# Kernel tuning notes

Measured on AMD Instinct MI355X. Metric: run time of the kernel, lower is better.

Reference implementation:

```python
import jax, jax.numpy as jnp
import numpy as np
from jax import lax

B, T, D, H = 4, 4096, 1024, 8
DK, DV = 1024, 2048          # expand_k=1.0, expand_v=2.0
RANK, MAXL, LOOPD = 16, 8, 128  # lora_rank, max_loops, dim*loop_dim_fraction
THRESH = 0.99
EPS = 1e-6
GK_SCALE = 16.0              # GLA forget-gate temperature


def setup_inputs() -> dict:
    key = jax.random.key(0)
    ks = jax.random.split(key, 16)
    r = lambda i, shape, s=0.02: jax.random.normal(ks[i], shape, jnp.float32) * s
    return {
        "h": jax.random.normal(ks[0], (B, T, D), jnp.float32),
        "e": jax.random.normal(ks[1], (B, T, D), jnp.float32),
        "norm_w": jnp.ones((D,), jnp.float32),
        "out_norm_w": jnp.ones((D,), jnp.float32),
        "Wq": r(2, (D, DK)), "Wk": r(3, (D, DK)), "Wv": r(4, (D, DV)),
        "Wgk": r(5, (D, DK)), "Wg": r(6, (D, DV)), "Wo": r(7, (DV, D)),
        "lora_A": r(8, (MAXL, D, RANK)), "lora_B": r(9, (MAXL, RANK, D)),
        "inj_A": 0.9 * jnp.eye(D, dtype=jnp.float32) + r(10, (D, D)),
        "inj_B": r(11, (D, D)),
        "act_w": r(12, (D,)),
        "act_b": jnp.full((), -2.0, jnp.float32),  # gradual halting
        "loop_table": r(13, (MAXL, LOOPD)),
        "n_loops": 4,
    }


def rmsnorm(x, w):
    return x * lax.rsqrt(jnp.mean(x * x, axis=-1, keepdims=True) + EPS) * w


def gla(x, Wq, Wk, Wv, Wgk, Wg, Wo, num_heads):
    """Gated Linear Attention: data-dependent forget gates, linear-time recurrent scan."""
    b, t, d = x.shape
    dk, dv = Wq.shape[1], Wv.shape[1]
    dkh, dvh = dk // num_heads, dv // num_heads
    q = (x @ Wq).reshape(b, t, num_heads, dkh) * (dkh ** -0.5)
    k = (x @ Wk).reshape(b, t, num_heads, dkh)
    v = (x @ Wv).reshape(b, t, num_heads, dvh)
    # forget gate alpha in (0,1): exp(logsigmoid(gk)/16)
    alpha = jnp.exp(jax.nn.log_sigmoid(x @ Wgk) / GK_SCALE).reshape(b, t, num_heads, dkh)

    def step(S, qkva):  # S: (b, H, dkh, dvh)
        qt, kt, vt, at = qkva
        S = at[..., None] * S + kt[..., None] * vt[..., None, :]
        ot = jnp.einsum('bhk,bhkv->bhv', qt, S)
        return S, ot

    S0 = jnp.zeros((b, num_heads, dkh, dvh), x.dtype)
    xs = (jnp.swapaxes(q, 0, 1), jnp.swapaxes(k, 0, 1),
          jnp.swapaxes(v, 0, 1), jnp.swapaxes(alpha, 0, 1))
    _, o = lax.scan(step, S0, xs)                  # o: (t, b, H, dvh)
    o = jnp.swapaxes(o, 0, 1).reshape(b, t, dv)
    o = o * jax.nn.silu(x @ Wg)                    # output gate
    return o @ Wo


def reference(h, e, norm_w, out_norm_w, Wq, Wk, Wv, Wgk, Wg, Wo,
              lora_A, lora_B, inj_A, inj_B, act_w, act_b, loop_table, n_loops):
    b, t_len, d = h.shape
    halted = jnp.zeros((b, t_len), bool)
    cum = jnp.zeros((b, t_len), h.dtype)
    h_out = jnp.zeros_like(h)
    loopd = loop_table.shape[1]
    for t in range(n_loops):  # small fixed depth loop (structurally distinct LoRA/embed per t)
        # loop index embedding on first loopd channels
        h = h.at[..., :loopd].add(loop_table[t])
        h_norm = rmsnorm(h + e, norm_w)
        g = gla(h_norm, Wq, Wk, Wv, Wgk, Wg, Wo, H)   # dropout: eval mode (identity)
        g = g + (g @ lora_A[t]) @ lora_B[t]            # depth LoRA
        h = h @ inj_A.T + e @ inj_B.T + g              # LTI injection: A.h + B.e + gla
        # ACT halting accumulate
        p = jax.nn.sigmoid(h @ act_w + act_b)          # (b, t_len)
        running = ~halted
        p_eff = jnp.where(running, p, jnp.zeros_like(p))
        new_cum = cum + p_eff
        newly = running & (new_cum >= THRESH)
        w = jnp.where(newly, 1.0 - cum, p_eff)         # remainder for newly-halted
        h_out = h_out + w[..., None] * h
        cum = new_cum
        halted = halted | newly
    return rmsnorm(h_out, out_norm_w)
```

## Files before the change

### kernel.cpp

```cpp
#include <hip/hip_runtime.h>

#define BB 4
#define TT 4096
#define DD 1024
#define HH 8
#define DKK 1024
#define DVV 2048
#define MR (BB*TT)
#define DKH 128
#define DVH 256
#define NLOOPS 4
#define LCH 128
#define NCH (TT/LCH)
#define PADW 136

#define WS_NEED 595202048ull

__device__ __attribute__((aligned(256))) unsigned char g_ws[WS_NEED];

typedef __bf16 bf16x8 __attribute__((ext_vector_type(8)));
typedef float  f32x4  __attribute__((ext_vector_type(4)));

__device__ __forceinline__ unsigned short f2bfu(float f) {
    unsigned int u = __builtin_bit_cast(unsigned int, f);
    u += 0x7fffu + ((u >> 16) & 1u);
    return (unsigned short)(u >> 16);
}
__device__ __forceinline__ float bfu2f(unsigned short s) {
    unsigned int u = ((unsigned int)s) << 16;
    return __builtin_bit_cast(float, u);
}

__device__ __forceinline__ void gld_lds16(const void* g, void* l) {
    __builtin_amdgcn_global_load_lds(
        (__attribute__((address_space(1))) void*)const_cast<void*>(g),
        (__attribute__((address_space(3))) void*)l, 16, 0, 0);
}

__global__ __launch_bounds__(256) void k_transpose_bf16(
    const float* __restrict__ in, unsigned short* __restrict__ out, int K, int N)
{
    __shared__ float tile[64][65];
    int k0 = blockIdx.y * 64, n0 = blockIdx.x * 64;
    int tx = threadIdx.x & 63, ty = threadIdx.x >> 6;
    #pragma unroll
    for (int r = 0; r < 64; r += 4)
        tile[ty + r][tx] = in[(size_t)(k0 + ty + r) * N + n0 + tx];
    __syncthreads();
    #pragma unroll
    for (int r = 0; r < 64; r += 4)
        out[(size_t)(n0 + ty + r) * K + k0 + tx] = f2bfu(tile[tx][ty + r]);
}

__global__ __launch_bounds__(256) void k_convert_bf16(
    const float* __restrict__ in, unsigned short* __restrict__ out)
{
    size_t i = ((size_t)blockIdx.x * 256 + threadIdx.x) * 4;
    float4 v = *(const float4*)&in[i];
    ushort4 o = make_ushort4(f2bfu(v.x), f2bfu(v.y), f2bfu(v.z), f2bfu(v.w));
    *(ushort4*)&out[i] = o;
}

__global__ __launch_bounds__(256) void k_conv_injA(
    const float* __restrict__ in, unsigned short* __restrict__ out,
    float* __restrict__ diag)
{
    int idx = blockIdx.x * 256 + threadIdx.x;
    int i = idx >> 10, j = idx & 1023;
    float v = in[idx];
    if (i == j) { diag[i] = v; out[idx] = 0; }
    else        { out[idx] = f2bfu(v); }
}

__global__ __launch_bounds__(256) void k_prep(
    float* __restrict__ h, const float* __restrict__ e,
    const float* __restrict__ norm_w, const float* __restrict__ ltab,
    unsigned short* __restrict__ h_bf, unsigned short* __restrict__ xn_bf)
{
    int row = blockIdx.x, tid = threadIdx.x;
    size_t base = (size_t)row * DD + tid * 4;
    float4 hv = *(float4*)&h[base];
    if (tid < 32) {
        float4 lv = *(const float4*)&ltab[tid * 4];
        hv.x += lv.x; hv.y += lv.y; hv.z += lv.z; hv.w += lv.w;
        *(float4*)&h[base] = hv;
    }
    float4 ev = *(const float4*)&e[base];
    float sx = hv.x + ev.x, sy = hv.y + ev.y, sz = hv.z + ev.z, sw = hv.w + ev.w;
    float partial = sx*sx + sy*sy + sz*sz + sw*sw;
    __shared__ float red[256];
    red[tid] = partial; __syncthreads();
    for (int st = 128; st > 0; st >>= 1) {
        if (tid < st) red[tid] += red[tid + st];
        __syncthreads();
    }
    float rms = rsqrtf(red[0] * (1.0f / DD) + 1e-6f);
    float4 wv = *(const float4*)&norm_w[tid * 4];
    *(ushort4*)&xn_bf[base] = make_ushort4(
        f2bfu(sx * rms * wv.x), f2bfu(sy * rms * wv.y),
        f2bfu(sz * rms * wv.z), f2bfu(sw * rms * wv.w));
    *(ushort4*)&h_bf[base] = make_ushort4(f2bfu(hv.x), f2bfu(hv.y), f2bfu(hv.z), f2bfu(hv.w));
}

template<int EPI, int OUTBF, int HASADD, int HASDIAG>
__global__ __launch_bounds__(256) void k_gemm(
    const unsigned short* __restrict__ A, const unsigned short* __restrict__ Bt,
    void* __restrict__ outp, const float* __restrict__ addend,
    const float* __restrict__ hsrc, const float* __restrict__ diag,
    int N, int K, float escale)
{
    __shared__ unsigned short lsA[128 * 32];
    __shared__ unsigned short lsB[128 * 32];
    int tid = threadIdx.x, lane = tid & 63, wave = tid >> 6;
    int wm = wave >> 1, wn = wave & 1;
    int bm = blockIdx.y * 128, bn = blockIdx.x * 128;
    int lrow = lane >> 2, lcol = (lane & 3) * 8;

    f32x4 acc[4][4];
    #pragma unroll
    for (int i = 0; i < 4; ++i)
        #pragma unroll
        for (int j = 0; j < 4; ++j) {
            f32x4 z = {0.f, 0.f, 0.f, 0.f};
            acc[i][j] = z;
        }

    for (int k0 = 0; k0 < K; k0 += 32) {
        __syncthreads();
        #pragma unroll
        for (int r = 0; r < 2; ++r) {
            int row = r * 64 + wave * 16 + lrow;
            gld_lds16(A  + (size_t)(bm + row) * K + k0 + lcol, &lsA[row * 32 + lcol]);
            gld_lds16(Bt + (size_t)(bn + row) * K + k0 + lcol, &lsB[row * 32 + lcol]);
        }
        __syncthreads();
        int quad = lane >> 4, mr = lane & 15;
        bf16x8 av[4], bv[4];
        #pragma unroll
        for (int t2 = 0; t2 < 4; ++t2) {
            av[t2] = *(const bf16x8*)&lsA[(wm * 64 + t2 * 16 + mr) * 32 + quad * 8];
            bv[t2] = *(const bf16x8*)&lsB[(wn * 64 + t2 * 16 + mr) * 32 + quad * 8];
        }
        #pragma unroll
        for (int tm = 0; tm < 4; ++tm)
            #pragma unroll
            for (int tn = 0; tn < 4; ++tn)
                acc[tm][tn] = __builtin_amdgcn_mfma_f32_16x16x32_bf16(
                    av[tm], bv[tn], acc[tm][tn], 0, 0, 0);
    }

    int quad = lane >> 4, col = lane & 15;
    float* outf = (float*)outp;
    unsigned short* outb = (unsigned short*)outp;
    #pragma unroll
    for (int tm = 0; tm < 4; ++tm) {
        int gm0 = bm + wm * 64 + tm * 16 + quad * 4;
        #pragma unroll
        for (int tn = 0; tn < 4; ++tn) {
            int gn = bn + wn * 64 + tn * 16 + col;
            #pragma unroll
            for (int r = 0; r < 4; ++r) {
                float val = acc[tm][tn][r];
                if (EPI == 1) val *= escale;
                if (EPI == 2)
                    val = (fminf(val, 0.f) - log1pf(expf(-fabsf(val)))) * 0.0625f;
                size_t oi = (size_t)(gm0 + r) * N + gn;
                if (HASDIAG) val += hsrc[oi] * diag[gn];
                if (HASADD)  val += addend[oi];
                if (OUTBF) outb[oi] = f2bfu(val);
                else       outf[oi] = val;
            }
        }
    }
}

__global__ __launch_bounds__(128) void k_c1(
    const float* __restrict__ lg, unsigned short* __restrict__ q,
    unsigned short* __restrict__ kk, float* __restrict__ dLe)
{
    int chunk = blockIdx.x, bh = blockIdx.y;
    int b = bh >> 3, h = bh & 7;
    int i = threadIdx.x;
    size_t r0 = (size_t)b * TT + (size_t)chunk * LCH;
    float c = 0.f, e = 1.f;
    for (int t = 0; t < LCH; ++t) {
        size_t off = (r0 + t) * DKK + h * DKH + i;
        c += lg[off];
        e = __expf(c);
        float ei = __expf(-c);
        q[off] = f2bfu(bfu2f(q[off]) * e);
        kk[off] = f2bfu(bfu2f(kk[off]) * ei);
    }
    dLe[((size_t)chunk * 32 + bh) * DKH + i] = e;
}

__global__ __launch_bounds__(256, 1) void k_c2(
    const unsigned short* __restrict__ q, const unsigned short* __restrict__ kk,
    const unsigned short* __restrict__ v, unsigned short* __restrict__ ob,
    float* __restrict__ U)
{
    extern __shared__ unsigned short sm[];
    unsigned short* lQ  = sm;
    unsigned short* lK  = sm + LCH * PADW;
    unsigned short* lKT = sm + 2 * LCH * PADW;
    unsigned short* lVT = sm + 3 * LCH * PADW;

    int chunk = blockIdx.x, bh = blockIdx.y;
    int b = bh >> 3, h = bh & 7;
    int tid = threadIdx.x, lane = tid & 63, wave = tid >> 6;
    int wm = wave >> 1, wn = wave & 1;
    int quad = lane >> 4, mr = lane & 15;
    size_t r0 = (size_t)b * TT + (size_t)chunk * LCH;

    #pragma unroll
    for (int ps = 0; ps < 8; ++ps) {
        int idx = ps * 256 + tid;
        int row = idx >> 4, c8 = (idx & 15) * 8;
        size_t g = (r0 + row) * DKK + h * DKH + c8;
        *(int4*)&lQ[row * PADW + c8] = *(const int4*)&q[g];
        union { int4 w; unsigned short u[8]; } tmp;
        tmp.w = *(const int4*)&kk[g];
        *(int4*)&lK[row * PADW + c8] = tmp.w;
        #pragma unroll
        for (int u2 = 0; u2 < 8; ++u2)
            lKT[(c8 + u2) * PADW + row] = tmp.u[u2];
    }
    __syncthreads();

    f32x4 pa[4][4];
    #pragma unroll
    for (int i = 0; i < 4; ++i)
        #pragma unroll
        for (int j = 0; j < 4; ++j) { f32x4 z = {0,0,0,0}; pa[i][j] = z; }
    for (int k0 = 0; k0 < DKH; k0 += 32) {
        bf16x8 av[4], bv[4];
        #pragma unroll
        for (int t2 = 0; t2 < 4; ++t2) {
            av[t2] = *(const bf16x8*)&lQ[(wm * 64 + t2 * 16 + mr) * PADW + k0 + quad * 8];
            bv[t2] = *(const bf16x8*)&lK[(wn * 64 + t2 * 16 + mr) * PADW + k0 + quad * 8];
        }
        #pragma unroll
        for (int tm = 0; tm < 4; ++tm)
            #pragma unroll
            for (int tn = 0; tn < 4; ++tn)
                pa[tm][tn] = __builtin_amdgcn_mfma_f32_16x16x32_bf16(
                    av[tm], bv[tn], pa[tm][tn], 0, 0, 0);
    }
    __syncthreads();

    #pragma unroll
    for (int tm = 0; tm < 4; ++tm)
        #pragma unroll
        for (int tn = 0; tn < 4; ++tn)
            #pragma unroll
            for (int r = 0; r < 4; ++r) {
                int trow = wm * 64 + tm * 16 + quad * 4 + r;
                int scol = wn * 64 + tn * 16 + mr;
                float pv = (trow >= scol) ? pa[tm][tn][r] : 0.f;
                lQ[trow * PADW + scol] = f2bfu(pv);
            }
    #pragma unroll
    for (int ps = 0; ps < 8; ++ps) {
        int idx = ps * 256 + tid;
        int s = idx >> 4, j8 = (idx & 15) * 8;
        size_t g = (r0 + s) * DVV + h * DVH + j8;
        union { int4 w; unsigned short u[8]; } tmp;
        tmp.w = *(const int4*)&v[g];
        #pragma unroll
        for (int u2 = 0; u2 < 8; ++u2)
            lVT[(j8 + u2) * PADW + s] = tmp.u[u2];
    }
    __syncthreads();

    #pragma unroll 1
    for (int panel = 0; panel < 2; ++panel) {
        f32x4 oa[4][4], ua[4][4];
        #pragma unroll
        for (int i = 0; i < 4; ++i)
            #pragma unroll
            for (int j = 0; j < 4; ++j) { f32x4 z = {0,0,0,0}; oa[i][j] = z; ua[i][j] = z; }
        for (int k0 = 0; k0 < LCH; k0 += 32) {
            bf16x8 pv[4], kt[4], vb[4];
            #pragma unroll
            for (int t2 = 0; t2 < 4; ++t2) {
                pv[t2] = *(const bf16x8*)&lQ [(wm * 64 + t2 * 16 + mr) * PADW + k0 + quad * 8];
                kt[t2] = *(const bf16x8*)&lKT[(wm * 64 + t2 * 16 + mr) * PADW + k0 + quad * 8];
                vb[t2] = *(const bf16x8*)&lVT[(wn * 64 + t2 * 16 + mr) * PADW + k0 + quad * 8];
            }
            #pragma unroll
            for (int tm = 0; tm < 4; ++tm)
                #pragma unroll
                for (int tn = 0; tn < 4; ++tn) {
                    oa[tm][tn] = __builtin_amdgcn_mfma_f32_16x16x32_bf16(
                        pv[tm], vb[tn], oa[tm][tn], 0, 0, 0);
                    ua[tm][tn] = __builtin_amdgcn_mfma_f32_16x16x32_bf16(
                        kt[tm], vb[tn], ua[tm][tn], 0, 0, 0);
                }
        }
        #pragma unroll
        for (int tm = 0; tm < 4; ++tm)
            #pragma unroll
            for (int tn = 0; tn < 4; ++tn)
                #pragma unroll
                for (int r = 0; r < 4; ++r) {
                    int m_ = wm * 64 + tm * 16 + quad * 4 + r;
                    int j_ = panel * 128 + wn * 64 + tn * 16 + mr;
                    ob[(r0 + m_) * DVV + h * DVH + j_] = f2bfu(oa[tm][tn][r]);
                    U[(((size_t)chunk * 32 + bh) * DKH + m_) * DVH + j_] = ua[tm][tn][r];
                }
        __syncthreads();
        if (panel == 0) {
            #pragma unroll
            for (int ps = 0; ps < 8; ++ps) {
                int idx = ps * 256 + tid;
                int s = idx >> 4, j8 = (idx & 15) * 8;
                size_t g = (r0 + s) * DVV + h * DVH + 128 + j8;
                union { int4 w; unsigned short u[8]; } tmp;
                tmp.w = *(const int4*)&v[g];
                #pragma unroll
                for (int u2 = 0; u2 < 8; ++u2)
                    lVT[(j8 + u2) * PADW + s] = tmp.u[u2];
            }
            __syncthreads();
        }
    }
}

__global__ __launch_bounds__(256) void k_c3(
    float* __restrict__ U, const float* __restrict__ dLe)
{
    int gid = blockIdx.x * 256 + threadIdx.x;
    int bh = gid >> 13;
    int rem = gid & 8191;
    int i = rem >> 6, j4 = rem & 63;
    float4 S = make_float4(0.f, 0.f, 0.f, 0.f);
    for (int c = 0; c < NCH; ++c) {
        size_t off = (((size_t)c * 32 + bh) * DKH + i) * DVH + j4 * 4;
        float4 u = *(float4*)&U[off];
        *(float4*)&U[off] = S;
        float d = dLe[((size_t)c * 32 + bh) * DKH + i];
        S.x = d * (S.x + u.x); S.y = d * (S.y + u.y);
        S.z = d * (S.z + u.z); S.w = d * (S.w + u.w);
    }
}

__global__ __launch_bounds__(256, 1) void k_c4(
    const unsigned short* __restrict__ q, const float* __restrict__ S,
    unsigned short* __restrict__ ob)
{
    extern __shared__ unsigned short sm[];
    unsigned short* lQ  = sm;
    unsigned short* lST = sm + LCH * PADW;

    int chunk = blockIdx.x, bh = blockIdx.y;
    int b = bh >> 3, h = bh & 7;
    int tid = threadIdx.x, lane = tid & 63, wave = tid >> 6;
    int wm = wave >> 1, wn = wave & 1;
    int quad = lane >> 4, mr = lane & 15;
    size_t r0 = (size_t)b * TT + (size_t)chunk * LCH;

    #pragma unroll
    for (int ps = 0; ps < 8; ++ps) {
        int idx = ps * 256 + tid;
        int row = idx >> 4, c8 = (idx & 15) * 8;
        size_t g = (r0 + row) * DKK + h * DKH + c8;
        *(int4*)&lQ[row * PADW + c8] = *(const int4*)&q[g];
    }

    #pragma unroll 1
    for (int panel = 0; panel < 2; ++panel) {
        __syncthreads();
        #pragma unroll
        for (int ps = 0; ps < 16; ++ps) {
            int idx = ps * 256 + tid;
            int i = idx >> 5, j4 = idx & 31;
            float4 sv = *(const float4*)&S[(((size_t)chunk * 32 + bh) * DKH + i) * DVH
                                           + panel * 128 + j4 * 4];
            lST[(j4 * 4 + 0) * PADW + i] = f2bfu(sv.x);
            lST[(j4 * 4 + 1) * PADW + i] = f2bfu(sv.y);
            lST[(j4 * 4 + 2) * PADW + i] = f2bfu(sv.z);
            lST[(j4 * 4 + 3) * PADW + i] = f2bfu(sv.w);
        }
        __syncthreads();

        f32x4 oa[4][4];
        #pragma unroll
        for (int i = 0; i < 4; ++i)
            #pragma unroll
            for (int j = 0; j < 4; ++j) { f32x4 z = {0,0,0,0}; oa[i][j] = z; }
        for (int k0 = 0; k0 < DKH; k0 += 32) {
            bf16x8 av[4], bv[4];
            #pragma unroll
            for (int t2 = 0; t2 < 4; ++t2) {
                av[t2] = *(const bf16x8*)&lQ [(wm * 64 + t2 * 16 + mr) * PADW + k0 + quad * 8];
                bv[t2] = *(const bf16x8*)&lST[(wn * 64 + t2 * 16 + mr) * PADW + k0 + quad * 8];
            }
            #pragma unroll
            for (int tm = 0; tm < 4; ++tm)
                #pragma unroll
                for (int tn = 0; tn < 4; ++tn)
                    oa[tm][tn] = __builtin_amdgcn_mfma_f32_16x16x32_bf16(
                        av[tm], bv[tn], oa[tm][tn], 0, 0, 0);
        }
        #pragma unroll
        for (int tm = 0; tm < 4; ++tm)
            #pragma unroll
            for (int tn = 0; tn < 4; ++tn)
                #pragma unroll
                for (int r = 0; r < 4; ++r) {
                    int t_ = wm * 64 + tm * 16 + quad * 4 + r;
                    int j_ = panel * 128 + wn * 64 + tn * 16 + mr;
                    size_t oi = (r0 + t_) * DVV + h * DVH + j_;
                    ob[oi] = f2bfu(bfu2f(ob[oi]) + oa[tm][tn][r]);
                }
    }
}

__global__ __launch_bounds__(256) void k_gate(
    unsigned short* __restrict__ o0, const unsigned short* __restrict__ xg)
{
    size_t i = ((size_t)blockIdx.x * 256 + threadIdx.x) * 8;
    union { int4 v; unsigned short u[8]; } A, G, R;
    A.v = *(const int4*)&o0[i];
    G.v = *(const int4*)&xg[i];
    #pragma unroll
    for (int j = 0; j < 8; ++j) {
        float ov = bfu2f(A.u[j]);
        float xf = bfu2f(G.u[j]);
        float sg = xf / (1.f + expf(-xf));
        R.u[j] = f2bfu(ov * sg);
    }
    *(int4*)&o0[i] = R.v;
}

__global__ __launch_bounds__(256) void k_lora1(
    const float* __restrict__ G, const float* __restrict__ A, float* __restrict__ tmp)
{
    int row = blockIdx.x * 4 + (threadIdx.x >> 6);
    int lane = threadIdx.x & 63;
    float acc[16];
    #pragma unroll
    for (int r = 0; r < 16; ++r) acc[r] = 0.f;
    const float* grow = G + (size_t)row * DD;
    for (int k2 = lane; k2 < DD; k2 += 64) {
        float g = grow[k2];
        const float4* ar = (const float4*)(A + k2 * 16);
        float4 a0 = ar[0], a1 = ar[1], a2 = ar[2], a3 = ar[3];
        acc[0] = fmaf(g, a0.x, acc[0]);  acc[1] = fmaf(g, a0.y, acc[1]);
        acc[2] = fmaf(g, a0.z, acc[2]);  acc[3] = fmaf(g, a0.w, acc[3]);
        acc[4] = fmaf(g, a1.x, acc[4]);  acc[5] = fmaf(g, a1.y, acc[5]);
        acc[6] = fmaf(g, a1.z, acc[6]);  acc[7] = fmaf(g, a1.w, acc[7]);
        acc[8] = fmaf(g, a2.x, acc[8]);  acc[9] = fmaf(g, a2.y, acc[9]);
        acc[10] = fmaf(g, a2.z, acc[10]); acc[11] = fmaf(g, a2.w, acc[11]);
        acc[12] = fmaf(g, a3.x, acc[12]); acc[13] = fmaf(g, a3.y, acc[13]);
        acc[14] = fmaf(g, a3.z, acc[14]); acc[15] = fmaf(g, a3.w, acc[15]);
    }
    #pragma unroll
    for (int off = 32; off >= 1; off >>= 1)
        #pragma unroll
        for (int r = 0; r < 16; ++r) acc[r] += __shfl_xor(acc[r], off);
    if (lane == 0) {
        #pragma unroll
        for (int r = 0; r < 16; ++r) tmp[(size_t)row * 16 + r] = acc[r];
    }
}

__global__ __launch_bounds__(256) void k_lora2(
    float* __restrict__ G, const float* __restrict__ tmp, const float* __restrict__ Bm)
{
    int row = blockIdx.x, tid = threadIdx.x;
    __shared__ float t16[16];
    if (tid < 16) t16[tid] = tmp[(size_t)row * 16 + tid];
    __syncthreads();
    size_t base = (size_t)row * DD + tid * 4;
    float4 acc = *(float4*)&G[base];
    #pragma unroll
    for (int r = 0; r < 16; ++r) {
        float tv = t16[r];
        float4 bv = *(const float4*)&Bm[r * DD + tid * 4];
        acc.x = fmaf(tv, bv.x, acc.x); acc.y = fmaf(tv, bv.y, acc.y);
        acc.z = fmaf(tv, bv.z, acc.z); acc.w = fmaf(tv, bv.w, acc.w);
    }
    *(float4*)&G[base] = acc;
}

__global__ __launch_bounds__(256) void k_act(
    const float* __restrict__ h, const float* __restrict__ act_w,
    const float* __restrict__ act_b, float* __restrict__ out,
    float* __restrict__ cum, int* __restrict__ halted)
{
    int row = blockIdx.x, tid = threadIdx.x;
    size_t base = (size_t)row * DD + tid * 4;
    float4 hv = *(const float4*)&h[base];
    float4 wv = *(const float4*)&act_w[tid * 4];
    float partial = hv.x*wv.x + hv.y*wv.y + hv.z*wv.z + hv.w*wv.w;
    __shared__ float red[256];
    __shared__ float s_cm;
    __shared__ int s_hl;
    if (tid == 0) { s_cm = cum[row]; s_hl = halted[row]; }
    red[tid] = partial; __syncthreads();
    for (int st = 128; st > 0; st >>= 1) {
        if (tid < st) red[tid] += red[tid + st];
        __syncthreads();
    }
    float p = 1.f / (1.f + expf(-(red[0] + act_b[0])));
    float cm = s_cm;
    int hl = s_hl;
    float p_eff = hl ? 0.f : p;
    float ncum = cm + p_eff;
    int newly = (!hl) && (ncum >= 0.99f);
    float w = newly ? (1.f - cm) : p_eff;
    float4 ho = *(float4*)&out[base];
    ho.x += w * hv.x; ho.y += w * hv.y; ho.z += w * hv.z; ho.w += w * hv.w;
    *(float4*)&out[base] = ho;
    if (tid == 0) { cum[row] = ncum; halted[row] = hl | newly; }
}

__global__ __launch_bounds__(256) void k_final(
    float* __restrict__ io, const float* __restrict__ w)
{
    int row = blockIdx.x, tid = threadIdx.x;
    size_t base = (size_t)row * DD + tid * 4;
    float4 hv = *(const float4*)&io[base];
    float partial = hv.x*hv.x + hv.y*hv.y + hv.z*hv.z + hv.w*hv.w;
    __shared__ float red[256];
    red[tid] = partial; __syncthreads();
    for (int st = 128; st > 0; st >>= 1) {
        if (tid < st) red[tid] += red[tid + st];
        __syncthreads();
    }
    float rms = rsqrtf(red[0] * (1.0f / DD) + 1e-6f);
    float4 wv = *(const float4*)&w[tid * 4];
    float4 o = make_float4(hv.x*rms*wv.x, hv.y*rms*wv.y, hv.z*rms*wv.z, hv.w*rms*wv.w);
    *(float4*)&io[base] = o;
}

extern "C" void kernel_launch(void* const* d_in, const int* in_sizes, int n_in,
                              void* d_out, int out_size, void* d_ws, size_t ws_size,
                              hipStream_t stream)
{
    const float* in_h       = (const float*)d_in[0];
    const float* in_e       = (const float*)d_in[1];
    const float* norm_w     = (const float*)d_in[2];
    const float* out_norm_w = (const float*)d_in[3];
    const float* Wq   = (const float*)d_in[4];
    const float* Wk   = (const float*)d_in[5];
    const float* Wv   = (const float*)d_in[6];
    const float* Wgk  = (const float*)d_in[7];
    const float* Wg   = (const float*)d_in[8];
    const float* Wo   = (const float*)d_in[9];
    const float* lora_A = (const float*)d_in[10];
    const float* lora_B = (const float*)d_in[11];
    const float* inj_A  = (const float*)d_in[12];
    const float* inj_B  = (const float*)d_in[13];
    const float* act_w  = (const float*)d_in[14];
    const float* act_b  = (const float*)d_in[15];
    const float* loop_table = (const float*)d_in[16];

    char* p;
    if (ws_size >= WS_NEED) {
        p = (char*)d_ws;
    } else {
        void* sym = nullptr;
        hipGetSymbolAddress(&sym, HIP_SYMBOL(g_ws));
        p = (char*)sym;
    }

    float* h      = (float*)p;            p += (size_t)MR * DD * 4;
    unsigned short* h_bf  = (unsigned short*)p; p += (size_t)MR * DD * 2;
    unsigned short* e_bf  = (unsigned short*)p; p += (size_t)MR * DD * 2;
    unsigned short* xn_bf = (unsigned short*)p; p += (size_t)MR * DD * 2;
    unsigned short* q_bf  = (unsigned short*)p; p += (size_t)MR * DKK * 2;
    unsigned short* k_bf  = (unsigned short*)p; p += (size_t)MR * DKK * 2;
    unsigned short* v_bf  = (unsigned short*)p; p += (size_t)MR * DVV * 2;
    float* lgbuf  = (float*)p;            p += (size_t)MR * DKK * 4;
    unsigned short* ob0   = (unsigned short*)p; p += (size_t)MR * DVV * 2;
    float* U      = (float*)p;            p += (size_t)NCH * 32 * DKH * DVH * 4;
    float* dLe    = (float*)p;            p += (size_t)NCH * 32 * DKH * 4;
    unsigned short* WqT  = (unsigned short*)p; p += (size_t)DKK * DD * 2;
    unsigned short* WkT  = (unsigned short*)p; p += (size_t)DKK * DD * 2;
    unsigned short* WgkT = (unsigned short*)p; p += (size_t)DKK * DD * 2;
    unsigned short* WvT  = (unsigned short*)p; p += (size_t)DVV * DD * 2;
    unsigned short* WgT  = (unsigned short*)p; p += (size_t)DVV * DD * 2;
    unsigned short* WoT  = (unsigned short*)p; p += (size_t)DD * DVV * 2;
    unsigned short* injA_bf = (unsigned short*)p; p += (size_t)DD * DD * 2;
    unsigned short* injB_bf = (unsigned short*)p; p += (size_t)DD * DD * 2;
    float* diagA = (float*)p;             p += DD * 4;
    float* tmp16 = (float*)p;             p += (size_t)MR * 16 * 4;
    float* cum   = (float*)p;             p += MR * 4;
    int*   halted = (int*)p;              p += MR * 4;
    unsigned short* xg_bf = q_bf;
    float* g2 = lgbuf;
    float* t1 = (float*)ob0;
    float* h_out = (float*)d_out;

    hipMemcpyAsync(h, in_h, (size_t)MR * DD * 4, hipMemcpyDeviceToDevice, stream);
    hipMemsetAsync(h_out, 0, (size_t)MR * DD * 4, stream);
    hipMemsetAsync(cum, 0, MR * 4, stream);
    hipMemsetAsync(halted, 0, MR * 4, stream);

    k_transpose_bf16<<<dim3(16, 16), 256, 0, stream>>>(Wq,  WqT,  DD, DKK);
    k_transpose_bf16<<<dim3(16, 16), 256, 0, stream>>>(Wk,  WkT,  DD, DKK);
    k_transpose_bf16<<<dim3(16, 16), 256, 0, stream>>>(Wgk, WgkT, DD, DKK);
    k_transpose_bf16<<<dim3(32, 16), 256, 0, stream>>>(Wv,  WvT,  DD, DVV);
    k_transpose_bf16<<<dim3(32, 16), 256, 0, stream>>>(Wg,  WgT,  DD, DVV);
    k_transpose_bf16<<<dim3(16, 32), 256, 0, stream>>>(Wo,  WoT,  DVV, DD);
    k_conv_injA<<<4096, 256, 0, stream>>>(inj_A, injA_bf, diagA);
    k_convert_bf16<<<1024, 256, 0, stream>>>(inj_B, injB_bf);
    k_convert_bf16<<<MR * DD / 1024, 256, 0, stream>>>(in_e, e_bf);

    const float qscale = 0.08838834764831845f;

    for (int t = 0; t < NLOOPS; ++t) {
        k_prep<<<MR, 256, 0, stream>>>(h, in_e, norm_w, loop_table + t * 128, h_bf, xn_bf);

        k_gemm<1,1,0,0><<<dim3(DKK/128, MR/128), 256, 0, stream>>>(
            xn_bf, WqT, q_bf, nullptr, nullptr, nullptr, DKK, DD, qscale);
        k_gemm<0,1,0,0><<<dim3(DKK/128, MR/128), 256, 0, stream>>>(
            xn_bf, WkT, k_bf, nullptr, nullptr, nullptr, DKK, DD, 1.f);
        k_gemm<2,0,0,0><<<dim3(DKK/128, MR/128), 256, 0, stream>>>(
            xn_bf, WgkT, lgbuf, nullptr, nullptr, nullptr, DKK, DD, 1.f);
        k_gemm<0,1,0,0><<<dim3(DVV/128, MR/128), 256, 0, stream>>>(
            xn_bf, WvT, v_bf, nullptr, nullptr, nullptr, DVV, DD, 1.f);

        k_c1<<<dim3(NCH, 32), 128, 0, stream>>>(lgbuf, q_bf, k_bf, dLe);
        k_c2<<<dim3(NCH, 32), 256, 4 * LCH * PADW * 2, stream>>>(
            q_bf, k_bf, v_bf, ob0, U);
        k_c3<<<1024, 256, 0, stream>>>(U, dLe);
        k_c4<<<dim3(NCH, 32), 256, 2 * LCH * PADW * 2, stream>>>(q_bf, U, ob0);

        k_gemm<0,1,0,0><<<dim3(DVV/128, MR/128), 256, 0, stream>>>(
            xn_bf, WgT, xg_bf, nullptr, nullptr, nullptr, DVV, DD, 1.f);

        k_gate<<<(int)((size_t)MR * DVV / 2048), 256, 0, stream>>>(ob0, xg_bf);

        k_gemm<0,0,0,0><<<dim3(DD/128, MR/128), 256, 0, stream>>>(
            ob0, WoT, g2, nullptr, nullptr, nullptr, DD, DVV, 1.f);

        k_lora1<<<MR / 4, 256, 0, stream>>>(g2, lora_A + (size_t)t * DD * 16, tmp16);
        k_lora2<<<MR, 256, 0, stream>>>(g2, tmp16, lora_B + (size_t)t * 16 * DD);

        k_gemm<0,0,1,1><<<dim3(DD/128, MR/128), 256, 0, stream>>>(
            h_bf, injA_bf, t1, g2, h, diagA, DD, DD, 1.f);
        k_gemm<0,0,1,0><<<dim3(DD/128, MR/128), 256, 0, stream>>>(
            e_bf, injB_bf, h, t1, nullptr, nullptr, DD, DD, 1.f);

        k_act<<<MR, 256, 0, stream>>>(h, act_w, act_b, h_out, cum, halted);
    }

    k_final<<<MR, 256, 0, stream>>>(h_out, out_norm_w);
}
```

Baseline: 5.047 ms.

## Merge projection GEMMs, concatenate injection GEMMs, fuse gate into chunk output, stage epilogues via LDS

The five input projections (q, k, gk, v, g) become one wide GEMM over a concatenated transposed weight, and each column block routes its output to the right buffer with the matching epilogue. The two injection GEMMs (A·h and B·e) become a single GEMM with K=2048 over a concatenated [h|e] activation and [injA|injB] weight, which drops the t1 intermediate round trip. The SiLU gate is folded into the k_c4 epilogue, and GEMM epilogues now stage tiles through shared memory so global stores are coalesced vector writes. This removes several launches and intermediate passes over memory, at the cost of extra workspace for a separate xg buffer and concatenated layouts.

```diff
diff --git a/kernel.cpp b/kernel.cpp
--- a/kernel.cpp
+++ b/kernel.cpp
@@ -13,13 +13,20 @@
 #define LCH 128
 #define NCH (TT/LCH)
 #define PADW 136
-
-#define WS_NEED 595202048ull
+#define NPROJ 7168
+
+#define WS_NEED 662310912ull
 
 __device__ __attribute__((aligned(256))) unsigned char g_ws[WS_NEED];
 
 typedef __bf16 bf16x8 __attribute__((ext_vector_type(8)));
 typedef float  f32x4  __attribute__((ext_vector_type(4)));
+
+union GemmSmem {
+    unsigned short ab[2][128 * 32];
+    unsigned short c16[128 * 136];
+    float cf[64 * 140];
+};
 
 __device__ __forceinline__ unsigned short f2bfu(float f) {
     unsigned int u = __builtin_bit_cast(unsigned int, f);
@@ -52,30 +59,35 @@
         out[(size_t)(n0 + ty + r) * K + k0 + tx] = f2bfu(tile[tx][ty + r]);
 }
 
-__global__ __launch_bounds__(256) void k_convert_bf16(
-    const float* __restrict__ in, unsigned short* __restrict__ out)
-{
-    size_t i = ((size_t)blockIdx.x * 256 + threadIdx.x) * 4;
-    float4 v = *(const float4*)&in[i];
-    ushort4 o = make_ushort4(f2bfu(v.x), f2bfu(v.y), f2bfu(v.z), f2bfu(v.w));
-    *(ushort4*)&out[i] = o;
-}
-
-__global__ __launch_bounds__(256) void k_conv_injA(
-    const float* __restrict__ in, unsigned short* __restrict__ out,
-    float* __restrict__ diag)
+__global__ __launch_bounds__(256) void k_conv_e(
+    const float* __restrict__ e, unsigned short* __restrict__ he)
+{
+    size_t gid = (size_t)blockIdx.x * 256 + threadIdx.x;
+    size_t b4 = gid * 4;
+    size_t row = b4 >> 10; int col = (int)(b4 & 1023);
+    float4 v = *(const float4*)&e[row * 1024 + col];
+    *(ushort4*)&he[row * 2048 + 1024 + col] =
+        make_ushort4(f2bfu(v.x), f2bfu(v.y), f2bfu(v.z), f2bfu(v.w));
+}
+
+__global__ __launch_bounds__(256) void k_conv_injcomb(
+    const float* __restrict__ injA, const float* __restrict__ injB,
+    unsigned short* __restrict__ WinjT, float* __restrict__ diag)
 {
     int idx = blockIdx.x * 256 + threadIdx.x;
     int i = idx >> 10, j = idx & 1023;
-    float v = in[idx];
-    if (i == j) { diag[i] = v; out[idx] = 0; }
-    else        { out[idx] = f2bfu(v); }
+    float va = injA[idx], vb = injB[idx];
+    unsigned short ua;
+    if (i == j) { diag[i] = va; ua = 0; }
+    else        { ua = f2bfu(va); }
+    WinjT[(size_t)i * 2048 + j] = ua;
+    WinjT[(size_t)i * 2048 + 1024 + j] = f2bfu(vb);
 }
 
 __global__ __launch_bounds__(256) void k_prep(
     float* __restrict__ h, const float* __restrict__ e,
     const float* __restrict__ norm_w, const float* __restrict__ ltab,
-    unsigned short* __restrict__ h_bf, unsigned short* __restrict__ xn_bf)
+    unsigned short* __restrict__ he, unsigned short* __restrict__ xn_bf)
 {
     int row = blockIdx.x, tid = threadIdx.x;
     size_t base = (size_t)row * DD + tid * 4;
@@ -99,31 +111,30 @@
     *(ushort4*)&xn_bf[base] = make_ushort4(
         f2bfu(sx * rms * wv.x), f2bfu(sy * rms * wv.y),
         f2bfu(sz * rms * wv.z), f2bfu(sw * rms * wv.w));
-    *(ushort4*)&h_bf[base] = make_ushort4(f2bfu(hv.x), f2bfu(hv.y), f2bfu(hv.z), f2bfu(hv.w));
-}
-
-template<int EPI, int OUTBF, int HASADD, int HASDIAG>
-__global__ __launch_bounds__(256) void k_gemm(
+    *(ushort4*)&he[(size_t)row * 2048 + tid * 4] =
+        make_ushort4(f2bfu(hv.x), f2bfu(hv.y), f2bfu(hv.z), f2bfu(hv.w));
+}
+
+__global__ __launch_bounds__(256) void k_gemm_proj(
     const unsigned short* __restrict__ A, const unsigned short* __restrict__ Bt,
-    void* __restrict__ outp, const float* __restrict__ addend,
-    const float* __restrict__ hsrc, const float* __restrict__ diag,
-    int N, int K, float escale)
-{
-    __shared__ unsigned short lsA[128 * 32];
-    __shared__ unsigned short lsB[128 * 32];
+    unsigned short* __restrict__ qout, unsigned short* __restrict__ kout,
+    float* __restrict__ lgout, unsigned short* __restrict__ vout,
+    unsigned short* __restrict__ xgout, float qscale)
+{
+    __shared__ GemmSmem sm;
+    unsigned short* lsA = sm.ab[0];
+    unsigned short* lsB = sm.ab[1];
     int tid = threadIdx.x, lane = tid & 63, wave = tid >> 6;
     int wm = wave >> 1, wn = wave & 1;
     int bm = blockIdx.y * 128, bn = blockIdx.x * 128;
     int lrow = lane >> 2, lcol = (lane & 3) * 8;
+    const int K = 1024;
 
     f32x4 acc[4][4];
     #pragma unroll
     for (int i = 0; i < 4; ++i)
         #pragma unroll
-        for (int j = 0; j < 4; ++j) {
-            f32x4 z = {0.f, 0.f, 0.f, 0.f};
-            acc[i][j] = z;
-        }
+        for (int j = 0; j < 4; ++j) { f32x4 z = {0,0,0,0}; acc[i][j] = z; }
 
     for (int k0 = 0; k0 < K; k0 += 32) {
         __syncthreads();
@@ -149,28 +160,140 @@
                     av[tm], bv[tn], acc[tm][tn], 0, 0, 0);
     }
 
-    int quad = lane >> 4, col = lane & 15;
-    float* outf = (float*)outp;
-    unsigned short* outb = (unsigned short*)outp;
-    #pragma unroll
-    for (int tm = 0; tm < 4; ++tm) {
-        int gm0 = bm + wm * 64 + tm * 16 + quad * 4;
-        #pragma unroll
-        for (int tn = 0; tn < 4; ++tn) {
-            int gn = bn + wn * 64 + tn * 16 + col;
-            #pragma unroll
-            for (int r = 0; r < 4; ++r) {
-                float val = acc[tm][tn][r];
-                if (EPI == 1) val *= escale;
-                if (EPI == 2)
-                    val = (fminf(val, 0.f) - log1pf(expf(-fabsf(val)))) * 0.0625f;
-                size_t oi = (size_t)(gm0 + r) * N + gn;
-                if (HASDIAG) val += hsrc[oi] * diag[gn];
-                if (HASADD)  val += addend[oi];
-                if (OUTBF) outb[oi] = f2bfu(val);
-                else       outf[oi] = val;
+    int quad = lane >> 4, mr = lane & 15;
+    __syncthreads();
+
+    if (bn >= 2048 && bn < 3072) {
+        int cb = bn - 2048;
+        #pragma unroll 1
+        for (int half = 0; half < 2; ++half) {
+            if (wm == half) {
+                #pragma unroll
+                for (int tm = 0; tm < 4; ++tm)
+                    #pragma unroll
+                    for (int tn = 0; tn < 4; ++tn)
+                        #pragma unroll
+                        for (int r = 0; r < 4; ++r) {
+                            float v = acc[tm][tn][r];
+                            v = (fminf(v, 0.f) - log1pf(expf(-fabsf(v)))) * 0.0625f;
+                            sm.cf[(tm * 16 + quad * 4 + r) * 140 + wn * 64 + tn * 16 + mr] = v;
+                        }
             }
-        }
+            __syncthreads();
+            #pragma unroll
+            for (int ps = 0; ps < 8; ++ps) {
+                int idx = ps * 256 + tid;
+                int rl = idx >> 5, c4 = (idx & 31) * 4;
+                float4 vv = *(float4*)&sm.cf[rl * 140 + c4];
+                *(float4*)&lgout[(size_t)(bm + half * 64 + rl) * 1024 + cb + c4] = vv;
+            }
+            __syncthreads();
+        }
+    } else {
+        unsigned short* obuf; int stride, cb;
+        float scale = 1.f;
+        if (bn < 1024)      { obuf = qout;  stride = 1024; cb = bn;        scale = qscale; }
+        else if (bn < 2048) { obuf = kout;  stride = 1024; cb = bn - 1024; }
+        else if (bn < 5120) { obuf = vout;  stride = 2048; cb = bn - 3072; }
+        else                { obuf = xgout; stride = 2048; cb = bn - 5120; }
+        #pragma unroll
+        for (int tm = 0; tm < 4; ++tm)
+            #pragma unroll
+            for (int tn = 0; tn < 4; ++tn)
+                #pragma unroll
+                for (int r = 0; r < 4; ++r)
+                    sm.c16[(wm * 64 + tm * 16 + quad * 4 + r) * 136
+                           + wn * 64 + tn * 16 + mr] = f2bfu(acc[tm][tn][r] * scale);
+        __syncthreads();
+        #pragma unroll
+        for (int ps = 0; ps < 8; ++ps) {
+            int idx = ps * 256 + tid;
+            int rl = idx >> 4, c8 = (idx & 15) * 8;
+            int4 w = *(int4*)&sm.c16[rl * 136 + c8];
+            *(int4*)&obuf[(size_t)(bm + rl) * stride + cb + c8] = w;
+        }
+    }
+}
+
+template<int HASADD, int HASDIAG>
+__global__ __launch_bounds__(256) void k_gemm_f32(
+    const unsigned short* __restrict__ A, const unsigned short* __restrict__ Bt,
+    float* __restrict__ out, const float* __restrict__ addend,
+    const float* __restrict__ hsrc, const float* __restrict__ diag,
+    int N, int K)
+{
+    __shared__ GemmSmem sm;
+    unsigned short* lsA = sm.ab[0];
+    unsigned short* lsB = sm.ab[1];
+    int tid = threadIdx.x, lane = tid & 63, wave = tid >> 6;
+    int wm = wave >> 1, wn = wave & 1;
+    int bm = blockIdx.y * 128, bn = blockIdx.x * 128;
+    int lrow = lane >> 2, lcol = (lane & 3) * 8;
+
+    f32x4 acc[4][4];
+    #pragma unroll
+    for (int i = 0; i < 4; ++i)
+        #pragma unroll
+        for (int j = 0; j < 4; ++j) { f32x4 z = {0,0,0,0}; acc[i][j] = z; }
+
+    for (int k0 = 0; k0 < K; k0 += 32) {
+        __syncthreads();
+        #pragma unroll
+        for (int r = 0; r < 2; ++r) {
+            int row = r * 64 + wave * 16 + lrow;
+            gld_lds16(A  + (size_t)(bm + row) * K + k0 + lcol, &lsA[row * 32 + lcol]);
+            gld_lds16(Bt + (size_t)(bn + row) * K + k0 + lcol, &lsB[row * 32 + lcol]);
+        }
+        __syncthreads();
+        int quad = lane >> 4, mr = lane & 15;
+        bf16x8 av[4], bv[4];
+        #pragma unroll
+        for (int t2 = 0; t2 < 4; ++t2) {
+            av[t2] = *(const bf16x8*)&lsA[(wm * 64 + t2 * 16 + mr) * 32 + quad * 8];
+            bv[t2] = *(const bf16x8*)&lsB[(wn * 64 + t2 * 16 + mr) * 32 + quad * 8];
+        }
+        #pragma unroll
+        for (int tm = 0; tm < 4; ++tm)
+            #pragma unroll
+            for (int tn = 0; tn < 4; ++tn)
+                acc[tm][tn] = __builtin_amdgcn_mfma_f32_16x16x32_bf16(
+                    av[tm], bv[tn], acc[tm][tn], 0, 0, 0);
+    }
+
+    int quad = lane >> 4, mr = lane & 15;
+    __syncthreads();
+    #pragma unroll 1
+    for (int half = 0; half < 2; ++half) {
+        if (wm == half) {
+            #pragma unroll
+            for (int tm = 0; tm < 4; ++tm)
+                #pragma unroll
+                for (int tn = 0; tn < 4; ++tn)
+                    #pragma unroll
+                    for (int r = 0; r < 4; ++r)
+                        sm.cf[(tm * 16 + quad * 4 + r) * 140
+                              + wn * 64 + tn * 16 + mr] = acc[tm][tn][r];
+        }
+        __syncthreads();
+        #pragma unroll
+        for (int ps = 0; ps < 8; ++ps) {
+            int idx = ps * 256 + tid;
+            int rl = idx >> 5, c4 = (idx & 31) * 4;
+            float4 vv = *(float4*)&sm.cf[rl * 140 + c4];
+            size_t oi = (size_t)(bm + half * 64 + rl) * N + bn + c4;
+            if (HASDIAG) {
+                float4 hh = *(const float4*)&hsrc[oi];
+                float4 dd = *(const float4*)&diag[bn + c4];
+                vv.x += hh.x * dd.x; vv.y += hh.y * dd.y;
+                vv.z += hh.z * dd.z; vv.w += hh.w * dd.w;
+            }
+            if (HASADD) {
+                float4 aa = *(const float4*)&addend[oi];
+                vv.x += aa.x; vv.y += aa.y; vv.z += aa.z; vv.w += aa.w;
+            }
+            *(float4*)&out[oi] = vv;
+        }
+        __syncthreads();
     }
 }
 
@@ -199,11 +322,11 @@
     const unsigned short* __restrict__ v, unsigned short* __restrict__ ob,
     float* __restrict__ U)
 {
-    extern __shared__ unsigned short sm[];
-    unsigned short* lQ  = sm;
-    unsigned short* lK  = sm + LCH * PADW;
-    unsigned short* lKT = sm + 2 * LCH * PADW;
-    unsigned short* lVT = sm + 3 * LCH * PADW;
+    extern __shared__ unsigned short smd[];
+    unsigned short* lQ  = smd;
+    unsigned short* lK  = smd + LCH * PADW;
+    unsigned short* lKT = smd + 2 * LCH * PADW;
+    unsigned short* lVT = smd + 3 * LCH * PADW;
 
     int chunk = blockIdx.x, bh = blockIdx.y;
     int b = bh >> 3, h = bh & 7;
@@ -346,11 +469,11 @@
 
 __global__ __launch_bounds__(256, 1) void k_c4(
     const unsigned short* __restrict__ q, const float* __restrict__ S,
-    unsigned short* __restrict__ ob)
-{
-    extern __shared__ unsigned short sm[];
-    unsigned short* lQ  = sm;
-    unsigned short* lST = sm + LCH * PADW;
+    unsigned short* __restrict__ ob, const unsigned short* __restrict__ xg)
+{
+    extern __shared__ unsigned short smd[];
+    unsigned short* lQ  = smd;
+    unsigned short* lST = smd + LCH * PADW;
 
     int chunk = blockIdx.x, bh = blockIdx.y;
     int b = bh >> 3, h = bh & 7;
@@ -411,26 +534,11 @@
                     int t_ = wm * 64 + tm * 16 + quad * 4 + r;
                     int j_ = panel * 128 + wn * 64 + tn * 16 + mr;
                     size_t oi = (r0 + t_) * DVV + h * DVH + j_;
-                    ob[oi] = f2bfu(bfu2f(ob[oi]) + oa[tm][tn][r]);
+                    float ov = bfu2f(ob[oi]) + oa[tm][tn][r];
+                    float xf = bfu2f(xg[oi]);
+                    ob[oi] = f2bfu(ov * xf / (1.f + expf(-xf)));
                 }
     }
-}
-
-__global__ __launch_bounds__(256) void k_gate(
-    unsigned short* __restrict__ o0, const unsigned short* __restrict__ xg)
-{
-    size_t i = ((size_t)blockIdx.x * 256 + threadIdx.x) * 8;
-    union { int4 v; unsigned short u[8]; } A, G, R;
-    A.v = *(const int4*)&o0[i];
-    G.v = *(const int4*)&xg[i];
-    #pragma unroll
-    for (int j = 0; j < 8; ++j) {
-        float ov = bfu2f(A.u[j]);
-        float xf = bfu2f(G.u[j]);
-        float sg = xf / (1.f + expf(-xf));
-        R.u[j] = f2bfu(ov * sg);
-    }
-    *(int4*)&o0[i] = R.v;
 }
 
 __global__ __launch_bounds__(256) void k_lora1(
@@ -567,31 +675,24 @@
     }
 
     float* h      = (float*)p;            p += (size_t)MR * DD * 4;
-    unsigned short* h_bf  = (unsigned short*)p; p += (size_t)MR * DD * 2;
-    unsigned short* e_bf  = (unsigned short*)p; p += (size_t)MR * DD * 2;
+    unsigned short* he_bf = (unsigned short*)p; p += (size_t)MR * 2048 * 2;
     unsigned short* xn_bf = (unsigned short*)p; p += (size_t)MR * DD * 2;
     unsigned short* q_bf  = (unsigned short*)p; p += (size_t)MR * DKK * 2;
     unsigned short* k_bf  = (unsigned short*)p; p += (size_t)MR * DKK * 2;
     unsigned short* v_bf  = (unsigned short*)p; p += (size_t)MR * DVV * 2;
+    unsigned short* xg_bf = (unsigned short*)p; p += (size_t)MR * DVV * 2;
     float* lgbuf  = (float*)p;            p += (size_t)MR * DKK * 4;
     unsigned short* ob0   = (unsigned short*)p; p += (size_t)MR * DVV * 2;
     float* U      = (float*)p;            p += (size_t)NCH * 32 * DKH * DVH * 4;
     float* dLe    = (float*)p;            p += (size_t)NCH * 32 * DKH * 4;
-    unsigned short* WqT  = (unsigned short*)p; p += (size_t)DKK * DD * 2;
-    unsigned short* WkT  = (unsigned short*)p; p += (size_t)DKK * DD * 2;
-    unsigned short* WgkT = (unsigned short*)p; p += (size_t)DKK * DD * 2;
-    unsigned short* WvT  = (unsigned short*)p; p += (size_t)DVV * DD * 2;
-    unsigned short* WgT  = (unsigned short*)p; p += (size_t)DVV * DD * 2;
-    unsigned short* WoT  = (unsigned short*)p; p += (size_t)DD * DVV * 2;
-    unsigned short* injA_bf = (unsigned short*)p; p += (size_t)DD * DD * 2;
-    unsigned short* injB_bf = (unsigned short*)p; p += (size_t)DD * DD * 2;
+    unsigned short* WprojT = (unsigned short*)p; p += (size_t)NPROJ * DKK * 2;
+    unsigned short* WoT    = (unsigned short*)p; p += (size_t)DD * DVV * 2;
+    unsigned short* WinjT  = (unsigned short*)p; p += (size_t)DD * 2048 * 2;
     float* diagA = (float*)p;             p += DD * 4;
     float* tmp16 = (float*)p;             p += (size_t)MR * 16 * 4;
     float* cum   = (float*)p;             p += MR * 4;
     int*   halted = (int*)p;              p += MR * 4;
-    unsigned short* xg_bf = q_bf;
     float* g2 = lgbuf;
-    float* t1 = (float*)ob0;
     float* h_out = (float*)d_out;
 
     hipMemcpyAsync(h, in_h, (size_t)MR * DD * 4, hipMemcpyDeviceToDevice, stream);
@@ -599,51 +700,37 @@
     hipMemsetAsync(cum, 0, MR * 4, stream);
     hipMemsetAsync(halted, 0, MR * 4, stream);
 
-    k_transpose_bf16<<<dim3(16, 16), 256, 0, stream>>>(Wq,  WqT,  DD, DKK);
-    k_transpose_bf16<<<dim3(16, 16), 256, 0, stream>>>(Wk,  WkT,  DD, DKK);
-    k_transpose_bf16<<<dim3(16, 16), 256, 0, stream>>>(Wgk, WgkT, DD, DKK);
-    k_transpose_bf16<<<dim3(32, 16), 256, 0, stream>>>(Wv,  WvT,  DD, DVV);
-    k_transpose_bf16<<<dim3(32, 16), 256, 0, stream>>>(Wg,  WgT,  DD, DVV);
-    k_transpose_bf16<<<dim3(16, 32), 256, 0, stream>>>(Wo,  WoT,  DVV, DD);
-    k_conv_injA<<<4096, 256, 0, stream>>>(inj_A, injA_bf, diagA);
-    k_convert_bf16<<<1024, 256, 0, stream>>>(inj_B, injB_bf);
-    k_convert_bf16<<<MR * DD / 1024, 256, 0, stream>>>(in_e, e_bf);
+    k_transpose_bf16<<<dim3(16, 16), 256, 0, stream>>>(Wq,  WprojT,              DD, DKK);
+    k_transpose_bf16<<<dim3(16, 16), 256, 0, stream>>>(Wk,  WprojT + 1024*1024,  DD, DKK);
+    k_transpose_bf16<<<dim3(16, 16), 256, 0, stream>>>(Wgk, WprojT + 2048*1024,  DD, DKK);
+    k_transpose_bf16<<<dim3(32, 16), 256, 0, stream>>>(Wv,  WprojT + 3072*1024,  DD, DVV);
+    k_transpose_bf16<<<dim3(32, 16), 256, 0, stream>>>(Wg,  WprojT + (size_t)5120*1024, DD, DVV);
+    k_transpose_bf16<<<dim3(16, 32), 256, 0, stream>>>(Wo,  WoT, DVV, DD);
+    k_conv_injcomb<<<4096, 256, 0, stream>>>(inj_A, inj_B, WinjT, diagA);
+    k_conv_e<<<MR * DD / 1024, 256, 0, stream>>>(in_e, he_bf);
 
     const float qscale = 0.08838834764831845f;
 
     for (int t = 0; t < NLOOPS; ++t) {
-        k_prep<<<MR, 256, 0, stream>>>(h, in_e, norm_w, loop_table + t * 128, h_bf, xn_bf);
-
-        k_gemm<1,1,0,0><<<dim3(DKK/128, MR/128), 256, 0, stream>>>(
-            xn_bf, WqT, q_bf, nullptr, nullptr, nullptr, DKK, DD, qscale);
-        k_gemm<0,1,0,0><<<dim3(DKK/128, MR/128), 256, 0, stream>>>(
-            xn_bf, WkT, k_bf, nullptr, nullptr, nullptr, DKK, DD, 1.f);
-        k_gemm<2,0,0,0><<<dim3(DKK/128, MR/128), 256, 0, stream>>>(
-            xn_bf, WgkT, lgbuf, nullptr, nullptr, nullptr, DKK, DD, 1.f);
-        k_gemm<0,1,0,0><<<dim3(DVV/128, MR/128), 256, 0, stream>>>(
-            xn_bf, WvT, v_bf, nullptr, nullptr, nullptr, DVV, DD, 1.f);
+        k_prep<<<MR, 256, 0, stream>>>(h, in_e, norm_w, loop_table + t * 128, he_bf, xn_bf);
+
+        k_gemm_proj<<<dim3(NPROJ/128, MR/128), 256, 0, stream>>>(
+            xn_bf, WprojT, q_bf, k_bf, lgbuf, v_bf, xg_bf, qscale);
 
         k_c1<<<dim3(NCH, 32), 128, 0, stream>>>(lgbuf, q_bf, k_bf, dLe);
         k_c2<<<dim3(NCH, 32), 256, 4 * LCH * PADW * 2, stream>>>(
             q_bf, k_bf, v_bf, ob0, U);
         k_c3<<<1024, 256, 0, stream>>>(U, dLe);
-        k_c4<<<dim3(NCH, 32), 256, 2 * LCH * PADW * 2, stream>>>(q_bf, U, ob0);
-
-        k_gemm<0,1,0,0><<<dim3(DVV/128, MR/128), 256, 0, stream>>>(
-            xn_bf, WgT, xg_bf, nullptr, nullptr, nullptr, DVV, DD, 1.f);
-
-        k_gate<<<(int)((size_t)MR * DVV / 2048), 256, 0, stream>>>(ob0, xg_bf);
-
-        k_gemm<0,0,0,0><<<dim3(DD/128, MR/128), 256, 0, stream>>>(
-            ob0, WoT, g2, nullptr, nullptr, nullptr, DD, DVV, 1.f);
+        k_c4<<<dim3(NCH, 32), 256, 2 * LCH * PADW * 2, stream>>>(q_bf, U, ob0, xg_bf);
+
+        k_gemm_f32<0,0><<<dim3(DD/128, MR/128), 256, 0, stream>>>(
+            ob0, WoT, g2, nullptr, nullptr, nullptr, DD, DVV);
 
         k_lora1<<<MR / 4, 256, 0, stream>>>(g2, lora_A + (size_t)t * DD * 16, tmp16);
         k_lora2<<<MR, 256, 0, stream>>>(g2, tmp16, lora_B + (size_t)t * 16 * DD);
 
-        k_gemm<0,0,1,1><<<dim3(DD/128, MR/128), 256, 0, stream>>>(
-            h_bf, injA_bf, t1, g2, h, diagA, DD, DD, 1.f);
-        k_gemm<0,0,1,0><<<dim3(DD/128, MR/128), 256, 0, stream>>>(
-            e_bf, injB_bf, h, t1, nullptr, nullptr, DD, DD, 1.f);
+        k_gemm_f32<1,1><<<dim3(DD/128, MR/128), 256, 0, stream>>>(
+            he_bf, WinjT, h, g2, h, diagA, DD, 2048);
 
         k_act<<<MR, 256, 0, stream>>>(h, act_w, act_b, h_out, cum, halted);
     }
```

New measurement: 4.834 ms. 1.04x faster.
